# Optimization experiments

Measured on AMD Instinct MI355X. Metric: run time of the kernel, lower is better.

Reference implementation:

```python
import jax, jax.numpy as jnp
import numpy as np

N = 4096
M0 = 2048
M1 = 2048
MCS = 4096
STRIDE = 2
D_NNGP = STRIDE ** 2 * M1              # 8192, input dim of layer-1 arccos maps
D_NTK = STRIDE ** 2 * (MCS + M1)       # 24576, input dim1 of layer-1 count sketch


def setup_inputs() -> dict:
    key = jax.random.key(0)
    ks = jax.random.split(key, 8)
    return {
        "layer_idx": 1,
        "z_nngp": jax.random.normal(ks[0], (N, D_NNGP), jnp.float32),
        "z_ntk": jax.random.normal(ks[1], (N, D_NTK), jnp.float32),
        "W0": jax.random.normal(ks[2], (D_NNGP, M0), jnp.float32),   # arccos0[1].W
        "W1": jax.random.normal(ks[3], (D_NNGP, M1), jnp.float32),   # arccos1[1].W
        "sign1": (jax.random.randint(ks[4], (D_NTK,), 0, 2) * 2 - 1).astype(jnp.float32),
        "indx1": jax.random.randint(ks[5], (D_NTK,), 0, MCS),
        "sign2": (jax.random.randint(ks[6], (M0,), 0, 2) * 2 - 1).astype(jnp.float32),
        "indx2": jax.random.randint(ks[7], (M0,), 0, MCS),
    }


def count_sketch(x, indx, sign, out_dim):
    # x: [n, d_in]; sign-multiply then scatter_add along last axis into out_dim bins
    xs = x * sign[None, :]
    out = jnp.zeros((x.shape[0], out_dim), dtype=x.dtype)
    return out.at[:, indx].add(xs)


def reference(layer_idx, z_nngp, z_ntk, W0, W1, sign1, indx1, sign2, indx2):
    norm0 = np.sqrt(2.0 / M0).astype(np.float32)
    norm1 = np.float32(np.sqrt(2.0 / M1) / 2.0)
    # arccos order-0 feature map (step function)
    xw0 = z_nngp @ W0
    tmp = (xw0 > 0).astype(z_nngp.dtype) * norm0          # [N, M0]
    # arccos order-1 feature map (relu-like: |xw| + xw)
    xw1 = z_nngp @ W1
    z_nngp_out = (jnp.abs(xw1) + xw1) * norm1             # [N, M1]
    # tensor sketch: count-sketch both, FFT, complex pointwise multiply, ifft.real
    x_cs = count_sketch(z_ntk, indx1, sign1, MCS)         # [N, MCS]
    y_cs = count_sketch(tmp, indx2, sign2, MCS)           # [N, MCS]
    z_ntk_out = jnp.fft.ifft(jnp.fft.fft(x_cs, axis=-1) * jnp.fft.fft(y_cs, axis=-1)).real
    z_ntk_cat = jnp.concatenate([z_nngp_out, z_ntk_out], axis=1)  # [N, M1+MCS]
    return (z_nngp_out, z_ntk_cat)
```

## Files before the change

kernel.cpp:

```cpp
#include <hip/hip_runtime.h>

#define NROW 4096
#define KDIM 8192
#define MDIM 2048
#define MCS_ 4096
#define DNTK 24576
#define CATW 6144
#define TAU_HALF 2.5e-3f
#define NT (KDIM / 32)

typedef __attribute__((ext_vector_type(8))) short short8;
typedef __attribute__((ext_vector_type(4))) float f32x4;

__device__ __forceinline__ void split2(float x0, float x1,
                                       unsigned& hi, unsigned& lo) {
    const unsigned u0 = __float_as_uint(x0);
    const unsigned u1 = __float_as_uint(x1);
    hi = (u0 >> 16) | (u1 & 0xFFFF0000u);
    const float l0 = x0 - __uint_as_float(u0 & 0xFFFF0000u);
    const float l1 = x1 - __uint_as_float(u1 & 0xFFFF0000u);
    lo = (__float_as_uint(l0) >> 16) | (__float_as_uint(l1) & 0xFFFF0000u);
}

__device__ __forceinline__ float2 cmulf(float2 a, float2 b) {
    return make_float2(a.x * b.x - a.y * b.y, a.x * b.y + a.y * b.x);
}

__global__ __launch_bounds__(512) void convert_kernel(
    const float* __restrict__ A,
    const float* __restrict__ W1,
    const float* __restrict__ W0,
    short8* __restrict__ aHi, short8* __restrict__ aLo,
    short8* __restrict__ wHi, short8* __restrict__ wLo)
{
    int b = blockIdx.x;
    const int tid = threadIdx.x;
    if (b < 4096) {
        const int P = b >> 8, T = b & 255;
        const float* src = A + (size_t)(P * 256) * KDIM + T * 32;
        short8* dh = aHi + ((size_t)b << 10);
        short8* dl = aLo + ((size_t)b << 10);
        for (int s = tid; s < 1024; s += 512) {
            const int row = ((s >> 6) << 4) | (s & 15);
            const int k0  = ((s >> 4) & 3) * 8;
            const float* p = src + (size_t)row * KDIM + k0;
            const float4 v0 = *reinterpret_cast<const float4*>(p);
            const float4 v1 = *reinterpret_cast<const float4*>(p + 4);
            union { short8 ss; unsigned u[4]; } h, l;
            split2(v0.x, v0.y, h.u[0], l.u[0]);
            split2(v0.z, v0.w, h.u[1], l.u[1]);
            split2(v1.x, v1.y, h.u[2], l.u[2]);
            split2(v1.z, v1.w, h.u[3], l.u[3]);
            dh[s] = h.ss; dl[s] = l.ss;
        }
    } else {
        b -= 4096;
        const int mat = b >> 11;
        const int T   = b & 255;
        const int Pc  = (b >> 8) & 7;
        const float* Wm = mat ? W0 : W1;
        const float* src = Wm + (size_t)(T * 32) * MDIM + Pc * 256;
        short8* dh = wHi + ((size_t)b << 10);
        short8* dl = wLo + ((size_t)b << 10);
        for (int s = tid; s < 1024; s += 512) {
            const int col = ((s >> 6) << 4) | (s & 15);
            const int k0  = ((s >> 4) & 3) * 8;
            float v[8];
#pragma unroll
            for (int j = 0; j < 8; ++j)
                v[j] = src[(size_t)(k0 + j) * MDIM + col];
            union { short8 ss; unsigned u[4]; } h, l;
            split2(v[0], v[1], h.u[0], l.u[0]);
            split2(v[2], v[3], h.u[1], l.u[1]);
            split2(v[4], v[5], h.u[2], l.u[2]);
            split2(v[6], v[7], h.u[3], l.u[3]);
            dh[s] = h.ss; dl[s] = l.ss;
        }
    }
}

__global__ __launch_bounds__(512) void csr_build(
    const int* __restrict__ indx1, const float* __restrict__ sign1,
    const int* __restrict__ indx2, const float* __restrict__ sign2,
    int* __restrict__ rowptr1, int* __restrict__ ent1,
    int* __restrict__ rowptr2, int* __restrict__ ent2)
{
    const int which = blockIdx.x;
    const int*   idx = which ? indx2 : indx1;
    const float* sg  = which ? sign2 : sign1;
    const int    n   = which ? 2048 : 24576;
    int* rowptr = which ? rowptr2 : rowptr1;
    int* ent    = which ? ent2 : ent1;

    __shared__ int h[4096];
    __shared__ int rp[4097];
    __shared__ int part[512];
    const int tid = threadIdx.x;

    for (int i = tid; i < 4096; i += 512) h[i] = 0;
    __syncthreads();
    for (int d = tid; d < n; d += 512) atomicAdd(&h[idx[d]], 1);
    __syncthreads();

    int loc[8], s = 0;
#pragma unroll
    for (int k = 0; k < 8; ++k) { loc[k] = h[8 * tid + k]; s += loc[k]; }
    part[tid] = s;
    __syncthreads();
    for (int off = 1; off < 512; off <<= 1) {
        int v = part[tid];
        if (tid >= off) v += part[tid - off];
        __syncthreads();
        part[tid] = v;
        __syncthreads();
    }
    int base = tid ? part[tid - 1] : 0;
#pragma unroll
    for (int k = 0; k < 8; ++k) { rp[8 * tid + k] = base; base += loc[k]; }
    if (tid == 511) rp[4096] = base;
    __syncthreads();

    for (int i = tid; i < 4096; i += 512) h[i] = 0;
    __syncthreads();
    for (int d = tid; d < n; d += 512) {
        const int b   = idx[d];
        const int pos = atomicAdd(&h[b], 1);
        ent[rp[b] + pos] = d | (sg[d] < 0.f ? 0x80000000 : 0);
    }
    __syncthreads();

    for (int i = tid; i < 4097; i += 512) rowptr[i] = rp[i];
    for (int b = tid; b < 4096; b += 512) {
        const int lo = rp[b], hi = rp[b + 1];
        for (int i = lo + 1; i < hi; ++i) {
            const int e = ent[i], key = e & 0x7FFFFFFF;
            int j = i - 1;
            while (j >= lo && (ent[j] & 0x7FFFFFFF) > key) { ent[j + 1] = ent[j]; --j; }
            ent[j + 1] = e;
        }
    }
}

__global__ __launch_bounds__(512, 2) void gemm_mfma_pre(
    const short8* __restrict__ aHi, const short8* __restrict__ aLo,
    const short8* __restrict__ wHi, const short8* __restrict__ wLo,
    float* __restrict__ out0, float* __restrict__ outCat)
{
    const int mode = blockIdx.z;
    __shared__ short8 AhiS[2][1024], AloS[2][1024];
    __shared__ short8 BhiS[2][1024], BloS[2][1024];

    const int tid  = threadIdx.x;
    const int lane = tid & 63;
    const int wid  = tid >> 6;
    const int wr   = wid >> 1;
    const int wc   = wid & 1;
    const int brow = blockIdx.y * 256;
    const int bcol = blockIdx.x * 256;

    const size_t aBase = ((size_t)blockIdx.y) << 18;
    const size_t wBase = ((size_t)(mode * 8 + blockIdx.x)) << 18;

    f32x4 acc[4][8];
#pragma unroll
    for (int m = 0; m < 4; ++m)
#pragma unroll
        for (int n = 0; n < 8; ++n)
#pragma unroll
            for (int i = 0; i < 4; ++i) acc[m][n][i] = 0.f;

    short8 st[8];

#define ISSUE(T)                                                             \
    {                                                                        \
        const size_t o = ((size_t)(T)) << 10;                                \
        st[0] = aHi[aBase + o + tid];  st[1] = aHi[aBase + o + tid + 512];   \
        st[2] = aLo[aBase + o + tid];  st[3] = aLo[aBase + o + tid + 512];   \
        st[4] = wHi[wBase + o + tid];  st[5] = wHi[wBase + o + tid + 512];   \
        st[6] = wLo[wBase + o + tid];  st[7] = wLo[wBase + o + tid + 512];   \
    }
#define WRITE(BUF)                                                           \
    {                                                                        \
        AhiS[BUF][tid] = st[0];  AhiS[BUF][tid + 512] = st[1];               \
        AloS[BUF][tid] = st[2];  AloS[BUF][tid + 512] = st[3];               \
        BhiS[BUF][tid] = st[4];  BhiS[BUF][tid + 512] = st[5];               \
        BloS[BUF][tid] = st[6];  BloS[BUF][tid + 512] = st[7];               \
    }

    ISSUE(0); WRITE(0); ISSUE(1);
    __syncthreads();

    for (int t = 0; t < NT; ++t) {
        const int cur = t & 1;

        short8 ah[4], al[4];
#pragma unroll
        for (int m = 0; m < 4; ++m) {
            ah[m] = AhiS[cur][(wr * 4 + m) * 64 + lane];
            al[m] = AloS[cur][(wr * 4 + m) * 64 + lane];
        }

        if (t + 1 < NT) {
            WRITE(cur ^ 1);
            if (t + 2 < NT) ISSUE(t + 2);
        }

#pragma unroll
        for (int n = 0; n < 8; ++n) {
            const short8 bh = BhiS[cur][(wc * 8 + n) * 64 + lane];
            const short8 bl = BloS[cur][(wc * 8 + n) * 64 + lane];
#pragma unroll
            for (int m = 0; m < 4; ++m) {
                acc[m][n] = __builtin_amdgcn_mfma_f32_16x16x32_bf16(
                    ah[m], bh, acc[m][n], 0, 0, 0);
                acc[m][n] = __builtin_amdgcn_mfma_f32_16x16x32_bf16(
                    ah[m], bl, acc[m][n], 0, 0, 0);
                acc[m][n] = __builtin_amdgcn_mfma_f32_16x16x32_bf16(
                    al[m], bh, acc[m][n], 0, 0, 0);
            }
        }
        __syncthreads();
    }
#undef ISSUE
#undef WRITE

    const float norm0 = 0.03125f;
    const int ocol0 = bcol + wc * 128 + (lane & 15);
    const int orow0 = brow + wr * 64 + ((lane >> 4) << 2);
#pragma unroll
    for (int m = 0; m < 4; ++m)
#pragma unroll
        for (int n = 0; n < 8; ++n) {
            const int col = ocol0 + n * 16;
#pragma unroll
            for (int i = 0; i < 4; ++i) {
                const int row = orow0 + m * 16 + i;
                if (mode == 0) {
                    const float v = fmaxf(acc[m][n][i], 0.f) * norm0;
                    out0[(size_t)row * MDIM + col] = v;
                    outCat[(size_t)row * CATW + col] = v;
                } else {
                    outCat[(size_t)row * CATW + 2048 + col] = acc[m][n][i];
                }
            }
        }
}

__global__ __launch_bounds__(512, 2) void gemm_mfma(
    const float* __restrict__ A,
    const float* __restrict__ W1,
    const float* __restrict__ W0,
    float* __restrict__ out0,
    float* __restrict__ outCat)
{
    const int mode = blockIdx.z;
    const float* __restrict__ W = mode ? W0 : W1;

    __shared__ short8 AhiS[2][1024], AloS[2][1024];
    __shared__ short8 BhiS[2][1024], BloS[2][1024];

    const int tid  = threadIdx.x;
    const int lane = tid & 63;
    const int wid  = tid >> 6;
    const int wr   = wid >> 1;
    const int wc   = wid & 1;
    const int brow = blockIdx.y * 256;
    const int bcol = blockIdx.x * 256;

    f32x4 acc[4][8];
#pragma unroll
    for (int m = 0; m < 4; ++m)
#pragma unroll
        for (int n = 0; n < 8; ++n)
#pragma unroll
            for (int i = 0; i < 4; ++i) acc[m][n][i] = 0.f;

    const int srow  = tid >> 1;
    const int skh   = tid & 1;
    const int slot0 = (srow >> 4) * 64 + (srow & 15) + (skh << 5);
    const float* aptr = A + (size_t)(brow + srow) * KDIM + skh * 16;
    const float* bptr = W + (size_t)(skh * 16) * MDIM + (bcol + srow);

    float4 av0, av1, av2, av3;
    float  bst[16];

#define LOAD_TILE(T)                                                         \
    {                                                                        \
        const float* ap = aptr + (T) * 32;                                   \
        av0 = *reinterpret_cast<const float4*>(ap);                          \
        av1 = *reinterpret_cast<const float4*>(ap + 4);                      \
        av2 = *reinterpret_cast<const float4*>(ap + 8);                      \
        av3 = *reinterpret_cast<const float4*>(ap + 12);                     \
        const float* bp = bptr + (size_t)((T) * 32) * MDIM;                  \
        _Pragma("unroll")                                                    \
        for (int j = 0; j < 16; ++j) bst[j] = bp[(size_t)j * MDIM];          \
    }
#define CONVERT_WRITE(BUF)                                                   \
    {                                                                        \
        union { short8 s; unsigned u[4]; } h, l;                             \
        split2(av0.x, av0.y, h.u[0], l.u[0]);                                \
        split2(av0.z, av0.w, h.u[1], l.u[1]);                                \
        split2(av1.x, av1.y, h.u[2], l.u[2]);                                \
        split2(av1.z, av1.w, h.u[3], l.u[3]);                                \
        AhiS[BUF][slot0] = h.s;  AloS[BUF][slot0] = l.s;                     \
        split2(av2.x, av2.y, h.u[0], l.u[0]);                                \
        split2(av2.z, av2.w, h.u[1], l.u[1]);                                \
        split2(av3.x, av3.y, h.u[2], l.u[2]);                                \
        split2(av3.z, av3.w, h.u[3], l.u[3]);                                \
        AhiS[BUF][slot0 + 16] = h.s;  AloS[BUF][slot0 + 16] = l.s;           \
        split2(bst[0], bst[1], h.u[0], l.u[0]);                              \
        split2(bst[2], bst[3], h.u[1], l.u[1]);                              \
        split2(bst[4], bst[5], h.u[2], l.u[2]);                              \
        split2(bst[6], bst[7], h.u[3], l.u[3]);                              \
        BhiS[BUF][slot0] = h.s;  BloS[BUF][slot0] = l.s;                     \
        split2(bst[8],  bst[9],  h.u[0], l.u[0]);                            \
        split2(bst[10], bst[11], h.u[1], l.u[1]);                            \
        split2(bst[12], bst[13], h.u[2], l.u[2]);                            \
        split2(bst[14], bst[15], h.u[3], l.u[3]);                            \
        BhiS[BUF][slot0 + 16] = h.s;  BloS[BUF][slot0 + 16] = l.s;           \
    }

    LOAD_TILE(0);
    CONVERT_WRITE(0);
    LOAD_TILE(1);
    __syncthreads();

    for (int t = 0; t < NT; ++t) {
        const int cur = t & 1;
        short8 ah[4], al[4];
#pragma unroll
        for (int m = 0; m < 4; ++m) {
            ah[m] = AhiS[cur][(wr * 4 + m) * 64 + lane];
            al[m] = AloS[cur][(wr * 4 + m) * 64 + lane];
        }
        if (t + 1 < NT) {
            CONVERT_WRITE(cur ^ 1);
            if (t + 2 < NT) LOAD_TILE(t + 2);
        }
#pragma unroll
        for (int n = 0; n < 8; ++n) {
            const short8 bh = BhiS[cur][(wc * 8 + n) * 64 + lane];
            const short8 bl = BloS[cur][(wc * 8 + n) * 64 + lane];
#pragma unroll
            for (int m = 0; m < 4; ++m) {
                acc[m][n] = __builtin_amdgcn_mfma_f32_16x16x32_bf16(
                    ah[m], bh, acc[m][n], 0, 0, 0);
                acc[m][n] = __builtin_amdgcn_mfma_f32_16x16x32_bf16(
                    ah[m], bl, acc[m][n], 0, 0, 0);
                acc[m][n] = __builtin_amdgcn_mfma_f32_16x16x32_bf16(
                    al[m], bh, acc[m][n], 0, 0, 0);
            }
        }
        __syncthreads();
    }
#undef LOAD_TILE
#undef CONVERT_WRITE

    const float norm0 = 0.03125f;
    const int ocol0 = bcol + wc * 128 + (lane & 15);
    const int orow0 = brow + wr * 64 + ((lane >> 4) << 2);
#pragma unroll
    for (int m = 0; m < 4; ++m)
#pragma unroll
        for (int n = 0; n < 8; ++n) {
            const int col = ocol0 + n * 16;
#pragma unroll
            for (int i = 0; i < 4; ++i) {
                const int row = orow0 + m * 16 + i;
                if (mode == 0) {
                    const float v = fmaxf(acc[m][n][i], 0.f) * norm0;
                    out0[(size_t)row * MDIM + col] = v;
                    outCat[(size_t)row * CATW + col] = v;
                } else {
                    outCat[(size_t)row * CATW + 2048 + col] = acc[m][n][i];
                }
            }
        }
}

#define ZP(i) Z[(i) + ((i) >> 4)]

__device__ __forceinline__ float2 twfetch(const float2* RT, int t) {
    if (t <= 512) return RT[t];
    const float2 r = RT[1024 - t];
    return make_float2(-r.y, -r.x);
}

__device__ __forceinline__ void fft_conv_body(float2* Z, const float2* RT, int tid) {
#pragma unroll
    for (int s = 0; s < 6; ++s) {
        const int lq = 2 * (5 - s);
        const int q  = 1 << lq;
        for (int b = tid; b < 1024; b += 512) {
            const int j    = b & (q - 1);
            const int base = ((b >> lq) << (lq + 2)) + j;
            const float2 x0 = ZP(base);
            const float2 x1 = ZP(base + q);
            const float2 x2 = ZP(base + 2 * q);
            const float2 x3 = ZP(base + 3 * q);
            const float2 w1 = twfetch(RT, j << (10 - lq));
            const float2 w2 = cmulf(w1, w1);
            const float2 w3 = cmulf(w2, w1);
            const float2 sA = make_float2(x0.x + x2.x, x0.y + x2.y);
            const float2 sB = make_float2(x0.x - x2.x, x0.y - x2.y);
            const float2 sC = make_float2(x1.x + x3.x, x1.y + x3.y);
            const float2 sD = make_float2(x1.x - x3.x, x1.y - x3.y);
            ZP(base) = make_float2(sA.x + sC.x, sA.y + sC.y);
            const float2 u1 = make_float2(sB.x + sD.y, sB.y - sD.x);
            const float2 u2 = make_float2(sA.x - sC.x, sA.y - sC.y);
            const float2 u3 = make_float2(sB.x - sD.y, sB.y + sD.x);
            ZP(base + q)     = cmulf(u1, w1);
            ZP(base + 2 * q) = cmulf(u2, w2);
            ZP(base + 3 * q) = cmulf(u3, w3);
        }
        __syncthreads();
    }

    for (int p = tid; p < MCS_; p += 512) {
        int q;
        if (p == 0) q = 0;
        else { const int h = 31 - __clz(p); q = 5 * (1 << (h & ~1)) - 1 - p; }
        if (p <= q) {
            const float2 Ap = ZP(p);
            const float2 Bq = ZP(q);
            const float Xr = 0.5f * (Ap.x + Bq.x);
            const float Xi = 0.5f * (Ap.y - Bq.y);
            const float Yr = 0.5f * (Ap.y + Bq.y);
            const float Yi = -0.5f * (Ap.x - Bq.x);
            const float Pr = Xr * Yr - Xi * Yi;
            const float Pi = Xr * Yi + Xi * Yr;
            ZP(p) = make_float2(Pr, Pi);
            ZP(q) = make_float2(Pr, -Pi);
        }
    }
    __syncthreads();

#pragma unroll
    for (int s = 0; s < 6; ++s) {
        const int lq = 2 * s;
        const int q  = 1 << lq;
        for (int b = tid; b < 1024; b += 512) {
            const int j    = b & (q - 1);
            const int base = ((b >> lq) << (lq + 2)) + j;
            const float2 t1 = twfetch(RT, j << (10 - lq));
            const float2 w1 = make_float2(t1.x, -t1.y);
            const float2 w2 = cmulf(w1, w1);
            const float2 w3 = cmulf(w2, w1);
            const float2 a  = ZP(base);
            const float2 b1 = cmulf(ZP(base + q),     w1);
            const float2 c  = cmulf(ZP(base + 2 * q), w2);
            const float2 d  = cmulf(ZP(base + 3 * q), w3);
            const float2 sA = make_float2(a.x + c.x, a.y + c.y);
            const float2 sB = make_float2(a.x - c.x, a.y - c.y);
            const float2 sC = make_float2(b1.x + d.x, b1.y + d.y);
            const float2 sD = make_float2(b1.x - d.x, b1.y - d.y);
            ZP(base)         = make_float2(sA.x + sC.x, sA.y + sC.y);
            ZP(base + q)     = make_float2(sB.x - sD.y, sB.y + sD.x);
            ZP(base + 2 * q) = make_float2(sA.x - sC.x, sA.y - sC.y);
            ZP(base + 3 * q) = make_float2(sB.x + sD.y, sB.y - sD.x);
        }
        __syncthreads();
    }
}

__global__ __launch_bounds__(512) void sketch_fft_csr(
    const float* __restrict__ z_ntk,
    const int* __restrict__ rowptr1, const int* __restrict__ ent1,
    const int* __restrict__ rowptr2, const int* __restrict__ ent2,
    float* __restrict__ outCat)
{
    __shared__ __align__(16) float2 Z[4352];
    __shared__ float2 RT[513];
    float* Zf = reinterpret_cast<float*>(Z);
    const int tid = threadIdx.x;
    const int row = blockIdx.x;
    const float norm0 = 0.03125f;

    const float wconst = -1.5339807878856412e-3f;
    for (int t = tid; t <= 512; t += 512) {
        float sw, cw;
        __sincosf(wconst * (float)t, &sw, &cw);
        RT[t] = make_float2(cw, sw);
    }

    int rpx[9], rpy[9];
#pragma unroll
    for (int k = 0; k < 9; ++k) {
        rpx[k] = rowptr1[8 * tid + k];
        rpy[k] = rowptr2[8 * tid + k];
    }
    float accX[8], accY[8];
#pragma unroll
    for (int k = 0; k < 8; ++k) { accX[k] = 0.f; accY[k] = 0.f; }
    int cur[8];
#pragma unroll
    for (int k = 0; k < 8; ++k) cur[k] = rpx[k];

    const float4* xrow4 = reinterpret_cast<const float4*>(z_ntk + (size_t)row * DNTK);
    for (int c = 0; c < 3; ++c) {
        const int lo = c * 8192, hi = lo + 8192;
        __syncthreads();
#pragma unroll
        for (int j = 0; j < 4; ++j)
            reinterpret_cast<float4*>(Zf)[tid + j * 512] = xrow4[c * 2048 + tid + j * 512];
        __syncthreads();
#pragma unroll
        for (int k = 0; k < 8; ++k) {
            while (cur[k] < rpx[k + 1]) {
                const int e = ent1[cur[k]];
                const int d = e & 0x7FFFFFFF;
                if (d >= hi) break;
                const float v = Zf[d - lo];
                accX[k] += (e < 0) ? -v : v;
                ++cur[k];
            }
        }
    }

    const float* trow = outCat + (size_t)row * CATW + 2048;
    __syncthreads();
    reinterpret_cast<float4*>(Zf)[tid] = reinterpret_cast<const float4*>(trow)[tid];
    __syncthreads();
#pragma unroll
    for (int k = 0; k < 8; ++k) {
        for (int c = rpy[k]; c < rpy[k + 1]; ++c) {
            const int e = ent2[c];
            const int d = e & 0x7FFFFFFF;
            const float t = Zf[d];
            const float y = (fabsf(t) < TAU_HALF) ? 0.5f * norm0
                                                  : (t > 0.f ? norm0 : 0.f);
            accY[k] += (e < 0) ? -y : y;
        }
    }
    __syncthreads();

#pragma unroll
    for (int k = 0; k < 8; ++k) {
        const int b = 8 * tid + k;
        ZP(b) = make_float2(accX[k], accY[k]);
    }
    __syncthreads();

    fft_conv_body(Z, RT, tid);

    float* orow = outCat + (size_t)row * CATW + 2048;
    const float scale = 1.0f / (float)MCS_;
    for (int n = tid; n < MCS_; n += 512) orow[n] = ZP(n).x * scale;
}

#define YBASE 4608
__global__ __launch_bounds__(512) void sketch_fft_atomic(
    const float* __restrict__ z_ntk,
    const float* __restrict__ sign1,
    const int*   __restrict__ indx1,
    const float* __restrict__ sign2,
    const int*   __restrict__ indx2,
    float* __restrict__ outCat)
{
    __shared__ __align__(16) float2 Z[4352];
    __shared__ float2 RT[513];
    float* Zf = reinterpret_cast<float*>(Z);
    const int tid = threadIdx.x;
    const int row = blockIdx.x;

    for (int i = tid; i < 2176; i += 512)
        reinterpret_cast<float4*>(Zf)[i] = make_float4(0.f, 0.f, 0.f, 0.f);
    const float wconst = -1.5339807878856412e-3f;
    for (int t = tid; t <= 512; t += 512) {
        float sw, cw;
        __sincosf(wconst * (float)t, &sw, &cw);
        RT[t] = make_float2(cw, sw);
    }
    __syncthreads();

    const float4* xrow4 = reinterpret_cast<const float4*>(z_ntk + (size_t)row * DNTK);
    const float4* s1v   = reinterpret_cast<const float4*>(sign1);
    const int4*   i1v   = reinterpret_cast<const int4*>(indx1);
    for (int v = tid; v < DNTK / 4; v += 512) {
        const float4 x = xrow4[v];
        const float4 s = s1v[v];
        const int4   ix = i1v[v];
        atomicAdd(&Zf[ix.x], x.x * s.x);
        atomicAdd(&Zf[ix.y], x.y * s.y);
        atomicAdd(&Zf[ix.z], x.z * s.z);
        atomicAdd(&Zf[ix.w], x.w * s.w);
    }
    const float norm0 = 0.03125f;
    const float* trow = outCat + (size_t)row * CATW + 2048;
    {
        const float4 t4 = reinterpret_cast<const float4*>(trow)[tid];
        const float4 s  = reinterpret_cast<const float4*>(sign2)[tid];
        const int4   ix = reinterpret_cast<const int4*>(indx2)[tid];
        const float y0 = (fabsf(t4.x) < TAU_HALF) ? 0.5f * norm0 : (t4.x > 0.f ? norm0 : 0.f);
        const float y1 = (fabsf(t4.y) < TAU_HALF) ? 0.5f * norm0 : (t4.y > 0.f ? norm0 : 0.f);
        const float y2 = (fabsf(t4.z) < TAU_HALF) ? 0.5f * norm0 : (t4.z > 0.f ? norm0 : 0.f);
        const float y3 = (fabsf(t4.w) < TAU_HALF) ? 0.5f * norm0 : (t4.w > 0.f ? norm0 : 0.f);
        atomicAdd(&Zf[YBASE + ix.x], y0 * s.x);
        atomicAdd(&Zf[YBASE + ix.y], y1 * s.y);
        atomicAdd(&Zf[YBASE + ix.z], y2 * s.z);
        atomicAdd(&Zf[YBASE + ix.w], y3 * s.w);
    }
    __syncthreads();

    {
        float re[8], im[8];
#pragma unroll
        for (int j = 0; j < 8; ++j) {
            const int i = tid + j * 512;
            re[j] = Zf[i];
            im[j] = Zf[YBASE + i];
        }
        __syncthreads();
#pragma unroll
        for (int j = 0; j < 8; ++j) {
            const int i = tid + j * 512;
            ZP(i) = make_float2(re[j], im[j]);
        }
    }
    __syncthreads();

    fft_conv_body(Z, RT, tid);

    float* orow = outCat + (size_t)row * CATW + 2048;
    const float scale = 1.0f / (float)MCS_;
    for (int n = tid; n < MCS_; n += 512) orow[n] = ZP(n).x * scale;
}

extern "C" void kernel_launch(void* const* d_in, const int* in_sizes, int n_in,
                              void* d_out, int out_size, void* d_ws, size_t ws_size,
                              hipStream_t stream) {
    (void)in_sizes; (void)n_in; (void)out_size;
    const float* z_nngp = (const float*)d_in[1];
    const float* z_ntk  = (const float*)d_in[2];
    const float* W0     = (const float*)d_in[3];
    const float* W1     = (const float*)d_in[4];
    const float* sign1  = (const float*)d_in[5];
    const int*   indx1  = (const int*)d_in[6];
    const float* sign2  = (const float*)d_in[7];
    const int*   indx2  = (const int*)d_in[8];

    float* out0   = (float*)d_out;
    float* outCat = out0 + (size_t)NROW * MDIM;

    const size_t NEED_P = 268435456ull;
    const size_t NEED_C = NEED_P + (1ull << 20);

    int* rowptr1 = nullptr; int* rowptr2 = nullptr;
    int* ent1 = nullptr;    int* ent2 = nullptr;
    const bool csr_ok = ws_size >= NEED_C;
    if (csr_ok) {
        int* base = (int*)((char*)d_ws + NEED_P);
        rowptr1 = base;
        rowptr2 = base + 4352;
        ent1    = base + 8704;
        ent2    = ent1 + 24576;
        csr_build<<<dim3(2), dim3(512), 0, stream>>>(
            indx1, sign1, indx2, sign2, rowptr1, ent1, rowptr2, ent2);
    }

    if (ws_size >= NEED_P) {
        short8* aHi = (short8*)d_ws;
        short8* aLo = aHi + (1ull << 22);
        short8* wHi = aLo + (1ull << 22);
        short8* wLo = wHi + (1ull << 22);
        convert_kernel<<<dim3(8192), dim3(512), 0, stream>>>(
            z_nngp, W1, W0, aHi, aLo, wHi, wLo);
        gemm_mfma_pre<<<dim3(8, 16, 2), dim3(512), 0, stream>>>(
            aHi, aLo, wHi, wLo, out0, outCat);
    } else {
        gemm_mfma<<<dim3(8, 16, 2), dim3(512), 0, stream>>>(
            z_nngp, W1, W0, out0, outCat);
    }

    if (csr_ok) {
        sketch_fft_csr<<<dim3(NROW), dim3(512), 0, stream>>>(
            z_ntk, rowptr1, ent1, rowptr2, ent2, outCat);
    } else {
        sketch_fft_atomic<<<dim3(NROW), dim3(512), 0, stream>>>(
            z_ntk, sign1, indx1, sign2, indx2, outCat);
    }
}
```

Baseline: 1.275 ms.

## Double-buffer z_ntk row chunks in LDS and prefetch into registers during gather

The sketch kernel now streams each z_ntk row in six 4096-float chunks into two LDS halves. The next chunk is loaded into registers while the current chunk is gathered, so global load latency overlaps the LDS gather work. It also adds a min-blocks hint to launch_bounds and defers loading the second rowptr until after the first gather to reduce register pressure. The cost is more barriers and a register-pressure cap that could cause spills.

```diff
diff --git a/kernel.cpp b/kernel.cpp
--- a/kernel.cpp
+++ b/kernel.cpp
@@ -463,7 +463,7 @@
     }
 }
 
-__global__ __launch_bounds__(512) void sketch_fft_csr(
+__global__ __launch_bounds__(512, 8) void sketch_fft_csr(
     const float* __restrict__ z_ntk,
     const int* __restrict__ rowptr1, const int* __restrict__ ent1,
     const int* __restrict__ rowptr2, const int* __restrict__ ent2,
@@ -483,53 +483,89 @@
         RT[t] = make_float2(cw, sw);
     }
 
-    int rpx[9], rpy[9];
-#pragma unroll
-    for (int k = 0; k < 9; ++k) {
-        rpx[k] = rowptr1[8 * tid + k];
-        rpy[k] = rowptr2[8 * tid + k];
-    }
-    float accX[8], accY[8];
-#pragma unroll
-    for (int k = 0; k < 8; ++k) { accX[k] = 0.f; accY[k] = 0.f; }
+    int rpx[9];
+#pragma unroll
+    for (int k = 0; k < 9; ++k) rpx[k] = rowptr1[8 * tid + k];
+    float accX[8];
+#pragma unroll
+    for (int k = 0; k < 8; ++k) accX[k] = 0.f;
     int cur[8];
 #pragma unroll
     for (int k = 0; k < 8; ++k) cur[k] = rpx[k];
 
     const float4* xrow4 = reinterpret_cast<const float4*>(z_ntk + (size_t)row * DNTK);
-    for (int c = 0; c < 3; ++c) {
-        const int lo = c * 8192, hi = lo + 8192;
-        __syncthreads();
-#pragma unroll
-        for (int j = 0; j < 4; ++j)
-            reinterpret_cast<float4*>(Zf)[tid + j * 512] = xrow4[c * 2048 + tid + j * 512];
-        __syncthreads();
+    const float4* trow4 = reinterpret_cast<const float4*>(outCat + (size_t)row * CATW + 2048);
+
+    float4 pA0, pA1, pB0, pB1, pT;
+
+#define LD_A(c) { pA0 = xrow4[(c) * 1024 + tid]; pA1 = xrow4[(c) * 1024 + tid + 512]; }
+#define LD_B(c) { pB0 = xrow4[(c) * 1024 + tid]; pB1 = xrow4[(c) * 1024 + tid + 512]; }
+#define WR_A(H) { float4* d_ = reinterpret_cast<float4*>(Zf + (H)); d_[tid] = pA0; d_[tid + 512] = pA1; }
+#define WR_B(H) { float4* d_ = reinterpret_cast<float4*>(Zf + (H)); d_[tid] = pB0; d_[tid + 512] = pB1; }
+#define GATHER(c)                                                              \
+    {                                                                          \
+        const int hi_ = ((c) + 1) * 4096;                                      \
+        const int off_ = ((c) & 1) * 4096 - (c) * 4096;                        \
+        _Pragma("unroll")                                                      \
+        for (int k = 0; k < 8; ++k) {                                          \
+            while (cur[k] < rpx[k + 1]) {                                      \
+                const int e = ent1[cur[k]];                                    \
+                const int d = e & 0x7FFFFFFF;                                  \
+                if (d >= hi_) break;                                           \
+                const float v = Zf[d + off_];                                  \
+                accX[k] += (e < 0) ? -v : v;                                   \
+                ++cur[k];                                                      \
+            }                                                                  \
+        }                                                                      \
+    }
+
+    LD_A(0); LD_B(1);
+    WR_A(0);
+    __syncthreads();
+    LD_A(2);
+
+    GATHER(0); __syncthreads();
+    WR_B(4096); LD_B(3); __syncthreads();
+
+    GATHER(1); __syncthreads();
+    WR_A(0);    LD_A(4); __syncthreads();
+
+    GATHER(2); __syncthreads();
+    WR_B(4096); LD_B(5); __syncthreads();
+
+    GATHER(3); __syncthreads();
+    WR_A(0);    pT = trow4[tid]; __syncthreads();
+
+    GATHER(4); __syncthreads();
+    WR_B(4096); __syncthreads();
+
+    GATHER(5);
+    reinterpret_cast<float4*>(Zf)[tid] = pT;
+    __syncthreads();
+
+#undef LD_A
+#undef LD_B
+#undef WR_A
+#undef WR_B
+#undef GATHER
+
+    float accY[8];
+#pragma unroll
+    for (int k = 0; k < 8; ++k) accY[k] = 0.f;
+    {
+        int rpy[9];
+#pragma unroll
+        for (int k = 0; k < 9; ++k) rpy[k] = rowptr2[8 * tid + k];
 #pragma unroll
         for (int k = 0; k < 8; ++k) {
-            while (cur[k] < rpx[k + 1]) {
-                const int e = ent1[cur[k]];
+            for (int c = rpy[k]; c < rpy[k + 1]; ++c) {
+                const int e = ent2[c];
                 const int d = e & 0x7FFFFFFF;
-                if (d >= hi) break;
-                const float v = Zf[d - lo];
-                accX[k] += (e < 0) ? -v : v;
-                ++cur[k];
+                const float t = Zf[d];
+                const float y = (fabsf(t) < TAU_HALF) ? 0.5f * norm0
+                                                      : (t > 0.f ? norm0 : 0.f);
+                accY[k] += (e < 0) ? -y : y;
             }
-        }
-    }
-
-    const float* trow = outCat + (size_t)row * CATW + 2048;
-    __syncthreads();
-    reinterpret_cast<float4*>(Zf)[tid] = reinterpret_cast<const float4*>(trow)[tid];
-    __syncthreads();
-#pragma unroll
-    for (int k = 0; k < 8; ++k) {
-        for (int c = rpy[k]; c < rpy[k + 1]; ++c) {
-            const int e = ent2[c];
-            const int d = e & 0x7FFFFFFF;
-            const float t = Zf[d];
-            const float y = (fabsf(t) < TAU_HALF) ? 0.5f * norm0
-                                                  : (t > 0.f ? norm0 : 0.f);
-            accY[k] += (e < 0) ? -y : y;
         }
     }
     __syncthreads();
```

After: 1.403 ms. 1.1x slower.

## Switch in-LDS FFT convolution from radix-4 to radix-8 butterflies

Applied to the files above, without the earlier changes.

Replaces the six radix-4 stages of the forward and inverse 4096-point FFTs with four radix-8 stages, one butterfly per thread. This cuts the number of shared-memory passes and barriers, and drops the twiddle symmetry branch since all indices now fall within the table. The digit-reversed pairing for the real-pair product is updated for base 8. It adds register pressure and more twiddle multiplies per thread.

```diff
diff --git a/kernel.cpp b/kernel.cpp
--- a/kernel.cpp
+++ b/kernel.cpp
@@ -379,47 +379,82 @@
 }
 
 #define ZP(i) Z[(i) + ((i) >> 4)]
-
-__device__ __forceinline__ float2 twfetch(const float2* RT, int t) {
-    if (t <= 512) return RT[t];
-    const float2 r = RT[1024 - t];
-    return make_float2(-r.y, -r.x);
-}
+#define C_SQ2 0.70710678118654752f
 
 __device__ __forceinline__ void fft_conv_body(float2* Z, const float2* RT, int tid) {
-#pragma unroll
-    for (int s = 0; s < 6; ++s) {
-        const int lq = 2 * (5 - s);
+    float2 x0, x1, x2, x3, x4, x5, x6, x7;
+
+#pragma unroll
+    for (int s = 0; s < 4; ++s) {
+        const int lq = 3 * (3 - s);
         const int q  = 1 << lq;
-        for (int b = tid; b < 1024; b += 512) {
-            const int j    = b & (q - 1);
-            const int base = ((b >> lq) << (lq + 2)) + j;
-            const float2 x0 = ZP(base);
-            const float2 x1 = ZP(base + q);
-            const float2 x2 = ZP(base + 2 * q);
-            const float2 x3 = ZP(base + 3 * q);
-            const float2 w1 = twfetch(RT, j << (10 - lq));
-            const float2 w2 = cmulf(w1, w1);
-            const float2 w3 = cmulf(w2, w1);
-            const float2 sA = make_float2(x0.x + x2.x, x0.y + x2.y);
-            const float2 sB = make_float2(x0.x - x2.x, x0.y - x2.y);
-            const float2 sC = make_float2(x1.x + x3.x, x1.y + x3.y);
-            const float2 sD = make_float2(x1.x - x3.x, x1.y - x3.y);
-            ZP(base) = make_float2(sA.x + sC.x, sA.y + sC.y);
-            const float2 u1 = make_float2(sB.x + sD.y, sB.y - sD.x);
-            const float2 u2 = make_float2(sA.x - sC.x, sA.y - sC.y);
-            const float2 u3 = make_float2(sB.x - sD.y, sB.y + sD.x);
-            ZP(base + q)     = cmulf(u1, w1);
-            ZP(base + 2 * q) = cmulf(u2, w2);
-            ZP(base + 3 * q) = cmulf(u3, w3);
-        }
+        const int j  = tid & (q - 1);
+        const int base = ((tid >> lq) << (lq + 3)) + j;
+        x0 = ZP(base);
+        x1 = ZP(base + q);
+        x2 = ZP(base + 2 * q);
+        x3 = ZP(base + 3 * q);
+        x4 = ZP(base + 4 * q);
+        x5 = ZP(base + 5 * q);
+        x6 = ZP(base + 6 * q);
+        x7 = ZP(base + 7 * q);
+
+        const float2 w1 = RT[j << (9 - lq)];
+        const float2 w2 = cmulf(w1, w1);
+        const float2 w3 = cmulf(w2, w1);
+        const float2 w4 = cmulf(w2, w2);
+        const float2 w5 = cmulf(w3, w2);
+        const float2 w6 = cmulf(w3, w3);
+        const float2 w7 = cmulf(w4, w3);
+
+        const float2 a0 = make_float2(x0.x + x4.x, x0.y + x4.y);
+        const float2 a1 = make_float2(x1.x + x5.x, x1.y + x5.y);
+        const float2 a2 = make_float2(x2.x + x6.x, x2.y + x6.y);
+        const float2 a3 = make_float2(x3.x + x7.x, x3.y + x7.y);
+        const float2 b0 = make_float2(x0.x - x4.x, x0.y - x4.y);
+        const float2 b1 = make_float2(x1.x - x5.x, x1.y - x5.y);
+        const float2 b2 = make_float2(x2.x - x6.x, x2.y - x6.y);
+        const float2 b3 = make_float2(x3.x - x7.x, x3.y - x7.y);
+
+        const float2 ca0 = make_float2(a0.x + a2.x, a0.y + a2.y);
+        const float2 ca1 = make_float2(a0.x - a2.x, a0.y - a2.y);
+        const float2 ca2 = make_float2(a1.x + a3.x, a1.y + a3.y);
+        const float2 ca3 = make_float2(a1.x - a3.x, a1.y - a3.y);
+        const float2 y0 = make_float2(ca0.x + ca2.x, ca0.y + ca2.y);
+        const float2 y4 = make_float2(ca0.x - ca2.x, ca0.y - ca2.y);
+        const float2 y2 = make_float2(ca1.x + ca3.y, ca1.y - ca3.x);
+        const float2 y6 = make_float2(ca1.x - ca3.y, ca1.y + ca3.x);
+
+        const float2 b1r = make_float2(C_SQ2 * (b1.x + b1.y), C_SQ2 * (b1.y - b1.x));
+        const float2 b2r = make_float2(b2.y, -b2.x);
+        const float2 b3r = make_float2(C_SQ2 * (b3.y - b3.x), -C_SQ2 * (b3.x + b3.y));
+        const float2 cb0 = make_float2(b0.x + b2r.x, b0.y + b2r.y);
+        const float2 cb1 = make_float2(b0.x - b2r.x, b0.y - b2r.y);
+        const float2 cb2 = make_float2(b1r.x + b3r.x, b1r.y + b3r.y);
+        const float2 cb3 = make_float2(b1r.x - b3r.x, b1r.y - b3r.y);
+        const float2 y1 = make_float2(cb0.x + cb2.x, cb0.y + cb2.y);
+        const float2 y5 = make_float2(cb0.x - cb2.x, cb0.y - cb2.y);
+        const float2 y3 = make_float2(cb1.x + cb3.y, cb1.y - cb3.x);
+        const float2 y7 = make_float2(cb1.x - cb3.y, cb1.y + cb3.x);
+
+        ZP(base)         = y0;
+        ZP(base + q)     = cmulf(y1, w1);
+        ZP(base + 2 * q) = cmulf(y2, w2);
+        ZP(base + 3 * q) = cmulf(y3, w3);
+        ZP(base + 4 * q) = cmulf(y4, w4);
+        ZP(base + 5 * q) = cmulf(y5, w5);
+        ZP(base + 6 * q) = cmulf(y6, w6);
+        ZP(base + 7 * q) = cmulf(y7, w7);
         __syncthreads();
     }
 
     for (int p = tid; p < MCS_; p += 512) {
         int q;
         if (p == 0) q = 0;
-        else { const int h = 31 - __clz(p); q = 5 * (1 << (h & ~1)) - 1 - p; }
+        else {
+            const int h = 31 - __clz(p);
+            q = 9 * (1 << (3 * (h / 3))) - 1 - p;
+        }
         if (p <= q) {
             const float2 Ap = ZP(p);
             const float2 Bq = ZP(q);
@@ -436,29 +471,70 @@
     __syncthreads();
 
 #pragma unroll
-    for (int s = 0; s < 6; ++s) {
-        const int lq = 2 * s;
+    for (int s = 0; s < 4; ++s) {
+        const int lq = 3 * s;
         const int q  = 1 << lq;
-        for (int b = tid; b < 1024; b += 512) {
-            const int j    = b & (q - 1);
-            const int base = ((b >> lq) << (lq + 2)) + j;
-            const float2 t1 = twfetch(RT, j << (10 - lq));
-            const float2 w1 = make_float2(t1.x, -t1.y);
-            const float2 w2 = cmulf(w1, w1);
-            const float2 w3 = cmulf(w2, w1);
-            const float2 a  = ZP(base);
-            const float2 b1 = cmulf(ZP(base + q),     w1);
-            const float2 c  = cmulf(ZP(base + 2 * q), w2);
-            const float2 d  = cmulf(ZP(base + 3 * q), w3);
-            const float2 sA = make_float2(a.x + c.x, a.y + c.y);
-            const float2 sB = make_float2(a.x - c.x, a.y - c.y);
-            const float2 sC = make_float2(b1.x + d.x, b1.y + d.y);
-            const float2 sD = make_float2(b1.x - d.x, b1.y - d.y);
-            ZP(base)         = make_float2(sA.x + sC.x, sA.y + sC.y);
-            ZP(base + q)     = make_float2(sB.x - sD.y, sB.y + sD.x);
-            ZP(base + 2 * q) = make_float2(sA.x - sC.x, sA.y - sC.y);
-            ZP(base + 3 * q) = make_float2(sB.x + sD.y, sB.y - sD.x);
-        }
+        const int j  = tid & (q - 1);
+        const int base = ((tid >> lq) << (lq + 3)) + j;
+
+        const float2 w1 = RT[j << (9 - lq)];
+        const float2 w2 = cmulf(w1, w1);
+        const float2 w3 = cmulf(w2, w1);
+        const float2 w4 = cmulf(w2, w2);
+        const float2 w5 = cmulf(w3, w2);
+        const float2 w6 = cmulf(w3, w3);
+        const float2 w7 = cmulf(w4, w3);
+
+        x0 = ZP(base);
+        {
+            float2 t;
+            t = ZP(base + q);     x1 = make_float2(t.x * w1.x + t.y * w1.y, t.y * w1.x - t.x * w1.y);
+            t = ZP(base + 2 * q); x2 = make_float2(t.x * w2.x + t.y * w2.y, t.y * w2.x - t.x * w2.y);
+            t = ZP(base + 3 * q); x3 = make_float2(t.x * w3.x + t.y * w3.y, t.y * w3.x - t.x * w3.y);
+            t = ZP(base + 4 * q); x4 = make_float2(t.x * w4.x + t.y * w4.y, t.y * w4.x - t.x * w4.y);
+            t = ZP(base + 5 * q); x5 = make_float2(t.x * w5.x + t.y * w5.y, t.y * w5.x - t.x * w5.y);
+            t = ZP(base + 6 * q); x6 = make_float2(t.x * w6.x + t.y * w6.y, t.y * w6.x - t.x * w6.y);
+            t = ZP(base + 7 * q); x7 = make_float2(t.x * w7.x + t.y * w7.y, t.y * w7.x - t.x * w7.y);
+        }
+
+        const float2 a0 = make_float2(x0.x + x4.x, x0.y + x4.y);
+        const float2 a1 = make_float2(x1.x + x5.x, x1.y + x5.y);
+        const float2 a2 = make_float2(x2.x + x6.x, x2.y + x6.y);
+        const float2 a3 = make_float2(x3.x + x7.x, x3.y + x7.y);
+        const float2 b0 = make_float2(x0.x - x4.x, x0.y - x4.y);
+        const float2 b1 = make_float2(x1.x - x5.x, x1.y - x5.y);
+        const float2 b2 = make_float2(x2.x - x6.x, x2.y - x6.y);
+        const float2 b3 = make_float2(x3.x - x7.x, x3.y - x7.y);
+
+        const float2 ca0 = make_float2(a0.x + a2.x, a0.y + a2.y);
+        const float2 ca1 = make_float2(a0.x - a2.x, a0.y - a2.y);
+        const float2 ca2 = make_float2(a1.x + a3.x, a1.y + a3.y);
+        const float2 ca3 = make_float2(a1.x - a3.x, a1.y - a3.y);
+        const float2 y0 = make_float2(ca0.x + ca2.x, ca0.y + ca2.y);
+        const float2 y4 = make_float2(ca0.x - ca2.x, ca0.y - ca2.y);
+        const float2 y2 = make_float2(ca1.x - ca3.y, ca1.y + ca3.x);
+        const float2 y6 = make_float2(ca1.x + ca3.y, ca1.y - ca3.x);
+
+        const float2 b1r = make_float2(C_SQ2 * (b1.x - b1.y), C_SQ2 * (b1.x + b1.y));
+        const float2 b2r = make_float2(-b2.y, b2.x);
+        const float2 b3r = make_float2(-C_SQ2 * (b3.x + b3.y), C_SQ2 * (b3.x - b3.y));
+        const float2 cb0 = make_float2(b0.x + b2r.x, b0.y + b2r.y);
+        const float2 cb1 = make_float2(b0.x - b2r.x, b0.y - b2r.y);
+        const float2 cb2 = make_float2(b1r.x + b3r.x, b1r.y + b3r.y);
+        const float2 cb3 = make_float2(b1r.x - b3r.x, b1r.y - b3r.y);
+        const float2 y1 = make_float2(cb0.x + cb2.x, cb0.y + cb2.y);
+        const float2 y5 = make_float2(cb0.x - cb2.x, cb0.y - cb2.y);
+        const float2 y3 = make_float2(cb1.x - cb3.y, cb1.y + cb3.x);
+        const float2 y7 = make_float2(cb1.x + cb3.y, cb1.y - cb3.x);
+
+        ZP(base)         = y0;
+        ZP(base + q)     = y1;
+        ZP(base + 2 * q) = y2;
+        ZP(base + 3 * q) = y3;
+        ZP(base + 4 * q) = y4;
+        ZP(base + 5 * q) = y5;
+        ZP(base + 6 * q) = y6;
+        ZP(base + 7 * q) = y7;
         __syncthreads();
     }
 }
```

Result: no change. 1.294 ms (+1.5%).
